# Optimization experiments

Hardware: AMD Instinct MI355X
Metric: run time of the kernel (lower is better)

## Reference

```python
import jax, jax.numpy as jnp
import numpy as np

K_NN = 9  # kernel_size: neighbors per node (includes self, dist 0)


def knn_edges(feat):
    """feat: (B, C, N). Replicates DenseDilatedKnnGraph (dilation=1):
    L2-normalize over channels, dense pairwise sq-distance, top-k nearest."""
    nrm = jnp.sqrt(jnp.sum(feat * feat, axis=1, keepdims=True))
    xn = feat / jnp.maximum(nrm, 1e-12)            # F.normalize(dim=1)
    xt = jnp.swapaxes(xn, 1, 2)                    # (B, N, C)
    sq = jnp.sum(xt * xt, axis=-1)                 # (B, N)
    dist = sq[:, :, None] + sq[:, None, :] - 2.0 * jnp.einsum('bnc,bmc->bnm', xt, xt)
    _, nn_idx = jax.lax.top_k(-dist, K_NN)         # (B, N, k)
    center = jnp.broadcast_to(jnp.arange(nn_idx.shape[1], dtype=nn_idx.dtype)[None, :, None], nn_idx.shape)
    return nn_idx, center                          # (x_j sources, x_i targets)


def reference(x, W0, W1, bias):
    B, C, H, W = x.shape
    N = H * W
    NB = B * N
    feat = x.reshape(B, C, N)
    # KNN graph is built on detached features in the torch source
    x_j, x_i = knn_edges(jax.lax.stop_gradient(feat))
    E = B * N * K_NN
    # faithful to source: torch.linspace(0, B, steps=E, dtype=int64) batch offsets
    count = jnp.linspace(0.0, float(B), E).astype(jnp.int32)
    src = x_j.reshape(-1).astype(jnp.int32) + count * N
    dst = x_i.reshape(-1).astype(jnp.int32) + count * N
    valid = (src < NB) & (dst < NB)                # drop the out-of-range tail edge
    # flat_nodes: (B, C, H, W) -> (B*H*W, C), node id = b*HW + pixel
    nodes = jnp.swapaxes(feat, 1, 2).reshape(NB, C)
    # ChebConv K=2, sym norm, lambda_max=2: Tx0 = x, Tx1 = -(D^-1/2 A D^-1/2) x
    w = valid.astype(nodes.dtype)
    deg = jax.ops.segment_sum(w, src, num_segments=NB)
    dinv = jnp.where(deg > 0, jax.lax.rsqrt(jnp.maximum(deg, 1.0)), 0.0)
    norm = -(dinv[src] * w * dinv[dst])            # scaled-Laplacian edge weights
    msg = norm[:, None] * nodes[src]               # (E, C) gather + weight
    Tx1 = jax.ops.segment_sum(msg, dst, num_segments=NB)
    return nodes @ W0 + Tx1 @ W1 + bias


def setup_inputs() -> dict:
    key = jax.random.key(0)
    k1, k2, k3, k4 = jax.random.split(key, 4)
    B, C, H, W = 8, 48, 64, 64
    Cout = 48
    s = 1.0 / np.sqrt(C)
    return {
        'x': jax.random.normal(k1, (B, C, H, W), dtype=jnp.float32),
        'W0': jax.random.normal(k2, (C, Cout), dtype=jnp.float32) * s,
        'W1': jax.random.normal(k3, (C, Cout), dtype=jnp.float32) * s,
        'bias': jax.random.normal(k4, (Cout,), dtype=jnp.float32) * 0.01,
    }
```

## Files before the change

kernel.cpp:

```cpp
#include <hip/hip_runtime.h>

#define BATCH 8
#define CH    48
#define NPTS  4096
#define NBN   (BATCH*NPTS)
#define KNN   9
#define NCAND 12

typedef unsigned short u16;
typedef unsigned int   u32;
typedef unsigned long long u64;
typedef __bf16 bf16x8 __attribute__((ext_vector_type(8)));
typedef float  f32x4  __attribute__((ext_vector_type(4)));

__device__ __forceinline__ float bf2f(u16 v) { return __uint_as_float(((u32)v) << 16); }
__device__ __forceinline__ u16 f2bf(float f) {
  u32 u = __float_as_uint(f);
  u = (u + 0x7fffu + ((u >> 16) & 1u)) >> 16;
  return (u16)u;
}

#define MED3U(d, a, b, c) \
  asm("v_med3_u32 %0, %1, %2, %3" : "=v"(d) : "v"(a), "v"(b), "v"(c))
#define INS12(p0,p1,p2,p3,p4,p5,p6,p7,p8,p9,p10,p11,x) do { \
  MED3U(p11,p10,p11,x); MED3U(p10,p9,p10,x); MED3U(p9,p8,p9,x);  \
  MED3U(p8, p7, p8, x); MED3U(p7, p6,p7, x); MED3U(p6,p5,p6,x);  \
  MED3U(p5, p4, p5, x); MED3U(p4, p3,p4, x); MED3U(p3,p2,p3,x);  \
  MED3U(p2, p1, p2, x); MED3U(p1, p0,p1, x); p0 = min(p0, x);    \
} while (0)

__device__ __forceinline__ void stage_q(const u16* g, u16* l) {
  __builtin_amdgcn_global_load_lds(
      (const __attribute__((address_space(1))) void*)g,
      (__attribute__((address_space(3))) void*)l, 16, 0, 0);
}

__global__ __launch_bounds__(256)
void k_prep(const float* __restrict__ x, float* __restrict__ xraw,
            float* __restrict__ xn, float* __restrict__ csq,
            u16* __restrict__ Abuf, u16* __restrict__ Bbuf,
            int* __restrict__ deg) {
  int node = blockIdx.x * 256 + threadIdx.x;
  deg[node] = 0;
  int b = node >> 12, n = node & (NPTS - 1);
  const float* xb = x + (size_t)b * CH * NPTS;
  float f[CH];
#pragma unroll
  for (int c = 0; c < CH; ++c) f[c] = xb[(size_t)c * NPTS + n];
  float a0 = 0, a1 = 0, a2 = 0, a3 = 0;
#pragma unroll
  for (int k = 0; k < CH; k += 4) {
    a0 += f[k] * f[k]; a1 += f[k+1] * f[k+1];
    a2 += f[k+2] * f[k+2]; a3 += f[k+3] * f[k+3];
  }
  float nrm = fmaxf(sqrtf((a0 + a1) + (a2 + a3)), 1e-12f);
  float xv[CH];
#pragma unroll
  for (int c = 0; c < CH; ++c) xv[c] = f[c] / nrm;
  a0 = a1 = a2 = a3 = 0;
#pragma unroll
  for (int k = 0; k < CH; k += 4) {
    a0 += xv[k] * xv[k]; a1 += xv[k+1] * xv[k+1];
    a2 += xv[k+2] * xv[k+2]; a3 += xv[k+3] * xv[k+3];
  }
  float csqv = (a0 + a1) + (a2 + a3);
  csq[node] = csqv;
  float4* ro = (float4*)(xraw + (size_t)node * CH);
  float4* no = (float4*)(xn   + (size_t)node * CH);
#pragma unroll
  for (int i = 0; i < CH / 4; ++i) {
    ro[i] = make_float4(f[4*i], f[4*i+1], f[4*i+2], f[4*i+3]);
    no[i] = make_float4(xv[4*i], xv[4*i+1], xv[4*i+2], xv[4*i+3]);
  }
  u16 ah[64], al[64];
#pragma unroll
  for (int k = 0; k < CH; ++k) {
    float av = -2.0f * xv[k];
    u16 h = f2bf(av); ah[k] = h; al[k] = f2bf(av - bf2f(h));
  }
  { u16 h = f2bf(csqv); ah[48] = h; al[48] = f2bf(csqv - bf2f(h)); }
#pragma unroll
  for (int k = 49; k < 64; ++k) { ah[k] = 0; al[k] = 0; }
  u16* Bh = Bbuf + (size_t)node * 128;
#pragma unroll
  for (int k = 0; k < CH; ++k) {
    float bv = xv[k];
    u16 h = f2bf(bv); Bh[k] = h; Bh[64 + k] = f2bf(bv - bf2f(h));
  }
  Bh[48] = 0x3F80; Bh[64 + 48] = 0;
#pragma unroll
  for (int k = 49; k < 64; ++k) { Bh[k] = 0; Bh[64 + k] = 0; }
  u16* Ag = Abuf + (size_t)(node >> 4) * 2048 + (size_t)(node & 15) * 8;
#pragma unroll
  for (int v = 0; v < 4; ++v) {
    const u16* src = (v < 2) ? ah : al;
    int koff = (v & 1) * 32;
#pragma unroll
    for (int q = 0; q < 4; ++q) {
      uint4 pk;
      const u16* s = src + koff + q * 8;
      pk.x = (u32)s[0] | ((u32)s[1] << 16);
      pk.y = (u32)s[2] | ((u32)s[3] << 16);
      pk.z = (u32)s[4] | ((u32)s[5] << 16);
      pk.w = (u32)s[6] | ((u32)s[7] << 16);
      *(uint4*)(Ag + v * 512 + q * 128) = pk;
    }
  }
}

__global__ __launch_bounds__(256, 6)
void k_knn_m(const u16* __restrict__ Abuf, const u16* __restrict__ Bbuf,
             u32* __restrict__ candu) {
  __shared__ __align__(16) u16 As[2][2048];
  int tid = threadIdx.x;
  int lane = tid & 63;
  int wv = tid >> 6;
  int quad = lane >> 4, m16 = lane & 15;
  int panel = blockIdx.x * 4 + wv;
  int row = panel * 16 + m16;
  int b4096 = row & ~(NPTS - 1);
  int quarter = blockIdx.y;
  int ct0 = quarter * 64;

  const __bf16* Bb = (const __bf16*)Bbuf + (size_t)row * 128;
  bf16x8 bh0 = *(const bf16x8*)(Bb + quad * 8);
  bf16x8 bh1 = *(const bf16x8*)(Bb + 32 + quad * 8);
  bf16x8 bl0 = *(const bf16x8*)(Bb + 64 + quad * 8);
  bf16x8 bl1 = *(const bf16x8*)(Bb + 96 + quad * 8);

  const u16* gs = Abuf + ((size_t)(b4096 >> 4) + ct0) * 2048
                  + wv * 512 + lane * 8;

  u32 s0=~0u,s1=~0u,s2=~0u,s3=~0u,s4=~0u,s5=~0u,
      s6=~0u,s7=~0u,s8=~0u,s9=~0u,s10=~0u,s11=~0u;

#define LDA(BUF, A0,A1,A2,A3) do {                                          \
    const u16* _p = &As[BUF][lane * 8];                                     \
    A0 = *(const bf16x8*)(_p);                                              \
    A1 = *(const bf16x8*)(_p + 512);                                        \
    A2 = *(const bf16x8*)(_p + 1024);                                       \
    A3 = *(const bf16x8*)(_p + 1536);                                       \
  } while (0)
#define MFMA6(ACC, A0,A1,A2,A3) do {                                        \
    ACC = (f32x4){2.5f, 2.5f, 2.5f, 2.5f};                                  \
    ACC = __builtin_amdgcn_mfma_f32_16x16x32_bf16(A0, bh0, ACC, 0, 0, 0);   \
    ACC = __builtin_amdgcn_mfma_f32_16x16x32_bf16(A1, bh1, ACC, 0, 0, 0);   \
    ACC = __builtin_amdgcn_mfma_f32_16x16x32_bf16(A0, bl0, ACC, 0, 0, 0);   \
    ACC = __builtin_amdgcn_mfma_f32_16x16x32_bf16(A1, bl1, ACC, 0, 0, 0);   \
    ACC = __builtin_amdgcn_mfma_f32_16x16x32_bf16(A2, bh0, ACC, 0, 0, 0);   \
    ACC = __builtin_amdgcn_mfma_f32_16x16x32_bf16(A3, bh1, ACC, 0, 0, 0);   \
  } while (0)
#define FILTER(ACC, CT) do {                                                \
    u32 _colb = ((u32)(CT) << 4) | ((u32)quad << 2);                        \
    _Pragma("unroll")                                                       \
    for (int _r = 0; _r < 4; ++_r) {                                        \
      u32 _u = __float_as_uint((ACC)[_r]);                                  \
      u32 _x = (_u & 0xFFFFF000u) | (_colb | (u32)_r);                      \
      INS12(s0,s1,s2,s3,s4,s5,s6,s7,s8,s9,s10,s11, _x);                     \
    }                                                                       \
  } while (0)

  f32x4 accA, accB;
  bf16x8 a0, a1, a2, a3;

  stage_q(gs, &As[0][wv * 512]);
  __syncthreads();

  LDA(0, a0, a1, a2, a3);
  stage_q(gs + (size_t)1 * 2048, &As[1][wv * 512]);
  MFMA6(accA, a0, a1, a2, a3);
  __syncthreads();

  for (int i = 0; i < 31; ++i) {
    int t = 2 * i + 1;
    LDA(1, a0, a1, a2, a3);
    stage_q(gs + (size_t)(t + 1) * 2048, &As[0][wv * 512]);
    FILTER(accA, ct0 + t - 1);
    MFMA6(accB, a0, a1, a2, a3);
    __syncthreads();
    LDA(0, a0, a1, a2, a3);
    stage_q(gs + (size_t)(t + 2) * 2048, &As[1][wv * 512]);
    FILTER(accB, ct0 + t);
    MFMA6(accA, a0, a1, a2, a3);
    __syncthreads();
  }
  LDA(1, a0, a1, a2, a3);
  FILTER(accA, ct0 + 62);
  MFMA6(accB, a0, a1, a2, a3);
  FILTER(accB, ct0 + 63);
#undef LDA
#undef MFMA6
#undef FILTER

  u32* o = candu + (((size_t)row * 4 + quarter) * 4 + quad) * NCAND;
  o[0]=s0; o[1]=s1; o[2]=s2; o[3]=s3; o[4]=s4; o[5]=s5;
  o[6]=s6; o[7]=s7; o[8]=s8; o[9]=s9; o[10]=s10; o[11]=s11;
}

__global__ __launch_bounds__(256, 4)
void k_reduce(const u32* __restrict__ candu, u32* __restrict__ cand12) {
  __shared__ u32 ls[64 * 4 * NCAND];
  int tid = threadIdx.x;
  int lr = tid >> 2, q = tid & 3;
  int row = blockIdx.x * 64 + lr;
  const u32* src = candu + (size_t)row * 192 + q * 48;
  u32 t0=~0u,t1=~0u,t2=~0u,t3=~0u,t4=~0u,t5=~0u,
      t6=~0u,t7=~0u,t8=~0u,t9=~0u,t10=~0u,t11=~0u;
  for (int s = 0; s < 48; ++s) {
    u32 x = src[s];
    INS12(t0,t1,t2,t3,t4,t5,t6,t7,t8,t9,t10,t11, x);
  }
  u32* lw = ls + (size_t)(lr * 4 + q) * NCAND;
  lw[0]=t0; lw[1]=t1; lw[2]=t2; lw[3]=t3; lw[4]=t4; lw[5]=t5;
  lw[6]=t6; lw[7]=t7; lw[8]=t8; lw[9]=t9; lw[10]=t10; lw[11]=t11;
  __syncthreads();
  if (q == 0) {
    u32 g0=~0u,g1=~0u,g2=~0u,g3=~0u,g4=~0u,g5=~0u,
        g6=~0u,g7=~0u,g8=~0u,g9=~0u,g10=~0u,g11=~0u;
    const u32* lsrc = ls + (size_t)lr * 48;
    for (int s = 0; s < 48; ++s) {
      u32 x = lsrc[s];
      INS12(g0,g1,g2,g3,g4,g5,g6,g7,g8,g9,g10,g11, x);
    }
    u32* o = cand12 + (size_t)row * NCAND;
    o[0]=(g0&0xFFFu); o[1]=(g1&0xFFFu); o[2]=(g2&0xFFFu);
    o[3]=(g3&0xFFFu); o[4]=(g4&0xFFFu); o[5]=(g5&0xFFFu);
    o[6]=(g6&0xFFFu); o[7]=(g7&0xFFFu); o[8]=(g8&0xFFFu);
    o[9]=(g9&0xFFFu); o[10]=(g10&0xFFFu); o[11]=(g11&0xFFFu);
  }
}

#define RR 16
__global__ __launch_bounds__(256, 4)
void k_rescore(const float* __restrict__ xn, const float* __restrict__ csq,
               const u32* __restrict__ cand12,
               u16* __restrict__ nn, int* __restrict__ deg) {
  __shared__ float dS[RR * NCAND];
  __shared__ int   iS[RR * NCAND];
  int tid = threadIdx.x;
  int lr = tid >> 4, q = tid & 15;
  int bi = blockIdx.x;
  int row = (bi & 7) * NPTS + (bi >> 3) * RR + lr;
  int b4096 = row & ~(NPTS - 1);
  const float* xnb = xn + (size_t)b4096 * CH;
  if (q < NCAND) {
    float rf[CH];
    const float4* p = (const float4*)(xn + (size_t)row * CH);
#pragma unroll
    for (int i = 0; i < CH / 4; ++i) {
      float4 v = p[i];
      rf[4*i] = v.x; rf[4*i+1] = v.y; rf[4*i+2] = v.z; rf[4*i+3] = v.w;
    }
    float sqn = csq[row];
    int c = (int)(cand12[(size_t)row * NCAND + q] & (NPTS - 1));
    const float4* cp = (const float4*)(xnb + (size_t)c * CH);
    float a0 = 0, a1 = 0, a2 = 0, a3 = 0;
#pragma unroll
    for (int i = 0; i < CH / 4; ++i) {
      float4 v = cp[i];
      a0 += rf[4*i]   * v.x; a1 += rf[4*i+1] * v.y;
      a2 += rf[4*i+2] * v.z; a3 += rf[4*i+3] * v.w;
    }
    float dist = (sqn + csq[b4096 + c]) - 2.0f * ((a0 + a1) + (a2 + a3));
    dS[lr * NCAND + q] = dist;
    iS[lr * NCAND + q] = c;
  }
  __syncthreads();
  if (q == 0) {
    float gd[KNN]; int gi[KNN];
#pragma unroll
    for (int j = 0; j < KNN; ++j) { gd[j] = 3.4e38f; gi[j] = 0x7fffffff; }
    for (int s = 0; s < NCAND; ++s) {
      float dc = dS[lr * NCAND + s]; int ic = iS[lr * NCAND + s];
      if (dc < gd[KNN - 1] || (dc == gd[KNN - 1] && ic < gi[KNN - 1])) {
        gd[KNN - 1] = dc; gi[KNN - 1] = ic;
#pragma unroll
        for (int k2 = KNN - 1; k2 > 0; --k2) {
          bool sw = (gd[k2] < gd[k2 - 1]) ||
                    (gd[k2] == gd[k2 - 1] && gi[k2] < gi[k2 - 1]);
          if (sw) {
            float td = gd[k2]; gd[k2] = gd[k2 - 1]; gd[k2 - 1] = td;
            int ti = gi[k2]; gi[k2] = gi[k2 - 1]; gi[k2 - 1] = ti;
          }
        }
      }
    }
    u16* o = nn + (size_t)row * KNN;
    int jmax = (row == NBN - 1) ? (KNN - 1) : KNN;
#pragma unroll
    for (int j = 0; j < KNN; ++j) o[j] = (u16)(gi[j] & (NPTS - 1));
    for (int j = 0; j < jmax; ++j)
      atomicAdd(&deg[b4096 + (gi[j] & (NPTS - 1))], 1);
  }
}

#define ONB 64
#define LPAD 52
__global__ __launch_bounds__(256)
void k_out_f(const float* __restrict__ xraw, const u16* __restrict__ nn,
             const int* __restrict__ deg,
             const float* __restrict__ W0, const float* __restrict__ W1,
             const float* __restrict__ bias, float* __restrict__ out) {
  __shared__ float w0[CH * CH], w1[CH * CH], bs[CH];
  __shared__ __align__(16) float fS[ONB * LPAD];
  __shared__ __align__(16) float txS[ONB * LPAD];
  __shared__ float dinvS[ONB];
  int tid = threadIdx.x;
  int bi = blockIdx.x;
  int n0 = (bi & 7) * NPTS + (bi >> 3) * ONB;
  int b12 = n0 & ~(NPTS - 1);
  for (int i = tid; i < CH * CH; i += 256) { w0[i] = W0[i]; w1[i] = W1[i]; }
  if (tid < CH) bs[tid] = bias[tid];
  for (int i = tid; i < ONB * 12; i += 256) {
    int ln = i / 12, f4 = i % 12;
    *(float4*)(fS + ln * LPAD + f4 * 4) =
        *(const float4*)(xraw + (size_t)(n0 + ln) * CH + f4 * 4);
  }
  if (tid < ONB) {
    int dg = deg[n0 + tid];
    dinvS[tid] = (dg > 0) ? (1.0f / sqrtf((float)dg)) : 0.0f;
  }
  __syncthreads();

  int ln = tid >> 2, p = tid & 3;
  int node = n0 + ln;
  float dn = dinvS[ln];
  const u16* nrow = nn + (size_t)node * KNN;
  bool full = (node != NBN - 1);
  float tx[12];
#pragma unroll
  for (int i = 0; i < 12; ++i) tx[i] = 0.f;
#pragma unroll
  for (int j = 0; j < KNN; ++j) {
    if (j < KNN - 1 || full) {
      int s = nrow[j] & (NPTS - 1);
      int dgs = deg[b12 + s];
      float ds = (dgs > 0) ? (1.0f / sqrtf((float)dgs)) : 0.0f;
      float w = -(ds * dn);
      const float4* pr = (const float4*)(xraw + (size_t)(b12 + s) * CH + p * 12);
#pragma unroll
      for (int q3 = 0; q3 < 3; ++q3) {
        float4 v = pr[q3];
        tx[q3*4]   += w * v.x; tx[q3*4+1] += w * v.y;
        tx[q3*4+2] += w * v.z; tx[q3*4+3] += w * v.w;
      }
    }
  }
#pragma unroll
  for (int q3 = 0; q3 < 3; ++q3)
    *(float4*)(txS + ln * LPAD + p * 12 + q3 * 4) =
        make_float4(tx[q3*4], tx[q3*4+1], tx[q3*4+2], tx[q3*4+3]);
  __syncthreads();

  float acc[12];
#pragma unroll
  for (int i = 0; i < 12; ++i) acc[i] = bs[p * 12 + i];
  const float* fr = fS + ln * LPAD;
  const float* tr = txS + ln * LPAD;
#pragma unroll
  for (int c = 0; c < CH; ++c) {
    float fc = fr[c];
    const float* wr = w0 + c * CH + p * 12;
#pragma unroll
    for (int i = 0; i < 12; ++i) acc[i] += fc * wr[i];
  }
#pragma unroll
  for (int c = 0; c < CH; ++c) {
    float tc = tr[c];
    const float* wr = w1 + c * CH + p * 12;
#pragma unroll
    for (int i = 0; i < 12; ++i) acc[i] += tc * wr[i];
  }
  float* op = out + (size_t)node * CH + p * 12;
#pragma unroll
  for (int q3 = 0; q3 < 3; ++q3)
    *(float4*)(op + q3 * 4) =
        make_float4(acc[q3*4], acc[q3*4+1], acc[q3*4+2], acc[q3*4+3]);
}

__global__ __launch_bounds__(256)
void k_zero(int* __restrict__ deg) { deg[blockIdx.x * 256 + threadIdx.x] = 0; }

__global__ __launch_bounds__(256)
void k_hist(const u16* __restrict__ nn, int* __restrict__ deg) {
  int node = blockIdx.x * 256 + threadIdx.x;
  int b12 = node & ~(NPTS - 1);
  int jmax = (node == NBN - 1) ? (KNN - 1) : KNN;
  for (int j = 0; j < jmax; ++j)
    atomicAdd(&deg[b12 + (nn[(size_t)node * KNN + j] & (NPTS - 1))], 1);
}

__global__ __launch_bounds__(256)
void k_dinv(const int* __restrict__ deg, float* __restrict__ dinv) {
  int i = blockIdx.x * 256 + threadIdx.x;
  int dg = deg[i];
  dinv[i] = (dg > 0) ? (1.0f / sqrtf((float)dg)) : 0.0f;
}

#define NQ    4
#define QCOLS (NPTS/NQ)
#define TCOLS 32
#define NTILES (QCOLS/TCOLS)
#define RPB   64

__global__ __launch_bounds__(256)
void k_knn_nb(const float* __restrict__ x, u16* __restrict__ nn) {
  __shared__ __align__(16) float tile[NQ * TCOLS * CH];
  __shared__ float nrmS[NQ * TCOLS];
  __shared__ float csq[NQ * TCOLS];
  int tid = threadIdx.x;
  int r0 = blockIdx.x * RPB;
  int b  = r0 >> 12;
  int q  = tid >> 6;
  int lr = tid & 63;
  int n  = (r0 + lr) & (NPTS - 1);
  const float* xb = x + (size_t)b * CH * NPTS;
  float rf[CH];
#pragma unroll
  for (int c = 0; c < CH; ++c) rf[c] = xb[(size_t)c * NPTS + n];
  float sqn;
  {
    float a0 = 0, a1 = 0, a2 = 0, a3 = 0;
#pragma unroll
    for (int k = 0; k < CH; k += 4) {
      a0 += rf[k] * rf[k]; a1 += rf[k+1] * rf[k+1];
      a2 += rf[k+2] * rf[k+2]; a3 += rf[k+3] * rf[k+3];
    }
    float nrm = fmaxf(sqrtf((a0 + a1) + (a2 + a3)), 1e-12f);
#pragma unroll
    for (int c = 0; c < CH; ++c) rf[c] = rf[c] / nrm;
    a0 = a1 = a2 = a3 = 0;
#pragma unroll
    for (int k = 0; k < CH; k += 4) {
      a0 += rf[k] * rf[k]; a1 += rf[k+1] * rf[k+1];
      a2 += rf[k+2] * rf[k+2]; a3 += rf[k+3] * rf[k+3];
    }
    sqn = (a0 + a1) + (a2 + a3);
  }
  float d[KNN]; int id[KNN];
#pragma unroll
  for (int j = 0; j < KNN; ++j) { d[j] = 3.4e38f; id[j] = 0x7fffffff; }
  for (int t = 0; t < NTILES; ++t) {
    __syncthreads();
#pragma unroll
    for (int qq = 0; qq < NQ; ++qq) {
      int colbase = qq * QCOLS + t * TCOLS;
      float* dst = tile + qq * TCOLS * CH;
#pragma unroll
      for (int it = 0; it < 6; ++it) {
        int i = it * 256 + tid;
        int c = i >> 5, p = i & 31;
        dst[p * CH + c] = xb[(size_t)c * NPTS + colbase + p];
      }
    }
    __syncthreads();
    if (tid < NQ * TCOLS) {
      const float* cp = tile + tid * CH;
      float a0 = 0, a1 = 0, a2 = 0, a3 = 0;
#pragma unroll
      for (int k = 0; k < CH; k += 4) {
        float4 v = *(const float4*)(cp + k);
        a0 += v.x * v.x; a1 += v.y * v.y; a2 += v.z * v.z; a3 += v.w * v.w;
      }
      nrmS[tid] = fmaxf(sqrtf((a0 + a1) + (a2 + a3)), 1e-12f);
    }
    __syncthreads();
    for (int i = tid; i < NQ * TCOLS * CH; i += 256)
      tile[i] = tile[i] / nrmS[i / CH];
    __syncthreads();
    if (tid < NQ * TCOLS) {
      const float* cp = tile + tid * CH;
      float a0 = 0, a1 = 0, a2 = 0, a3 = 0;
#pragma unroll
      for (int k = 0; k < CH; k += 4) {
        float4 v = *(const float4*)(cp + k);
        a0 += v.x * v.x; a1 += v.y * v.y; a2 += v.z * v.z; a3 += v.w * v.w;
      }
      csq[tid] = (a0 + a1) + (a2 + a3);
    }
    __syncthreads();
    int cbase = q * QCOLS + t * TCOLS;
    const float* tq = tile + q * TCOLS * CH;
    for (int cc = 0; cc < TCOLS; ++cc) {
      const float* cp = tq + cc * CH;
      float a0 = 0, a1 = 0, a2 = 0, a3 = 0;
#pragma unroll
      for (int k = 0; k < CH; k += 4) {
        float4 v = *(const float4*)(cp + k);
        a0 += rf[k] * v.x; a1 += rf[k+1] * v.y;
        a2 += rf[k+2] * v.z; a3 += rf[k+3] * v.w;
      }
      float dist = (sqn + csq[q * TCOLS + cc]) - 2.0f * ((a0 + a1) + (a2 + a3));
      if (dist < d[KNN - 1]) {
        d[KNN - 1] = dist; id[KNN - 1] = cbase + cc;
#pragma unroll
        for (int k2 = KNN - 1; k2 > 0; --k2) {
          if (d[k2] < d[k2 - 1]) {
            float td = d[k2]; d[k2] = d[k2 - 1]; d[k2 - 1] = td;
            int ti = id[k2]; id[k2] = id[k2 - 1]; id[k2 - 1] = ti;
          }
        }
      }
    }
  }
  __syncthreads();
  float* md = tile;
  int*   mi = (int*)(tile + 256 * KNN);
#pragma unroll
  for (int j = 0; j < KNN; ++j) { md[tid * KNN + j] = d[j]; mi[tid * KNN + j] = id[j]; }
  __syncthreads();
  if (tid < RPB) {
    float fd[KNN]; int fi[KNN];
#pragma unroll
    for (int j = 0; j < KNN; ++j) { fd[j] = 3.4e38f; fi[j] = 0x7fffffff; }
    for (int qq = 0; qq < NQ; ++qq) {
      int s = qq * RPB + tid;
      for (int j = 0; j < KNN; ++j) {
        float dc = md[s * KNN + j]; int ic = mi[s * KNN + j];
        if (dc < fd[KNN - 1]) {
          fd[KNN - 1] = dc; fi[KNN - 1] = ic;
#pragma unroll
          for (int k2 = KNN - 1; k2 > 0; --k2) {
            if (fd[k2] < fd[k2 - 1]) {
              float td = fd[k2]; fd[k2] = fd[k2 - 1]; fd[k2 - 1] = td;
              int ti = fi[k2]; fi[k2] = fi[k2 - 1]; fi[k2 - 1] = ti;
            }
          }
        }
      }
    }
    u16* o = nn + (size_t)(r0 + tid) * KNN;
#pragma unroll
    for (int j = 0; j < KNN; ++j) o[j] = (u16)(fi[j] & (NPTS - 1));
  }
}

__global__ __launch_bounds__(256)
void k_out_nb(const float* __restrict__ x, const u16* __restrict__ nn,
              const float* __restrict__ dinv,
              const float* __restrict__ W0, const float* __restrict__ W1,
              const float* __restrict__ bias, float* __restrict__ out) {
  __shared__ float w0[CH * CH], w1[CH * CH], bs[CH];
  for (int i = threadIdx.x; i < CH * CH; i += 256) { w0[i] = W0[i]; w1[i] = W1[i]; }
  if (threadIdx.x < CH) bs[threadIdx.x] = bias[threadIdx.x];
  __syncthreads();
  int node = blockIdx.x * 256 + threadIdx.x;
  int b = node >> 12, n = node & (NPTS - 1);
  const float* xb = x + (size_t)b * CH * NPTS;
  float f[CH], acc[CH], tx[CH];
#pragma unroll
  for (int c = 0; c < CH; ++c) f[c] = xb[(size_t)c * NPTS + n];
#pragma unroll
  for (int o = 0; o < CH; ++o) acc[o] = bs[o];
#pragma unroll
  for (int c = 0; c < CH; ++c) {
    float fc = f[c];
    const float* wr = w0 + c * CH;
#pragma unroll
    for (int o = 0; o < CH; ++o) acc[o] += fc * wr[o];
  }
#pragma unroll
  for (int c = 0; c < CH; ++c) tx[c] = 0.f;
  float dn = dinv[node];
  int jmax = (node == NBN - 1) ? (KNN - 1) : KNN;
  for (int j = 0; j < jmax; ++j) {
    int s = nn[(size_t)node * KNN + j] & (NPTS - 1);
    float w = -(dinv[(b << 12) + s] * dn);
#pragma unroll
    for (int c = 0; c < CH; ++c) tx[c] += w * xb[(size_t)c * NPTS + s];
  }
#pragma unroll
  for (int c = 0; c < CH; ++c) {
    float tc = tx[c];
    const float* wr = w1 + c * CH;
#pragma unroll
    for (int o = 0; o < CH; ++o) acc[o] += tc * wr[o];
  }
  float4* op = (float4*)(out + (size_t)node * CH);
#pragma unroll
  for (int i = 0; i < CH / 4; ++i)
    op[i] = make_float4(acc[4*i], acc[4*i+1], acc[4*i+2], acc[4*i+3]);
}

extern "C" void kernel_launch(void* const* d_in, const int* in_sizes, int n_in,
                              void* d_out, int out_size, void* d_ws, size_t ws_size,
                              hipStream_t stream) {
  const float* x    = (const float*)d_in[0];
  const float* W0   = (const float*)d_in[1];
  const float* W1   = (const float*)d_in[2];
  const float* bias = (const float*)d_in[3];
  float* out = (float*)d_out;
  char* w = (char*)d_ws;

  const size_t SZ_XN   = (size_t)NBN * CH * 4;
  const size_t SZ_XRAW = (size_t)NBN * CH * 4;
  const size_t SZ_CSQ  = (size_t)NBN * 4;
  const size_t SZ_NN   = (size_t)NBN * KNN * 2;
  const size_t SZ_DEG  = (size_t)NBN * 4;
  const size_t SZ_AB   = (size_t)NBN * 128 * 2;
  const size_t SZ_CU   = (size_t)NBN * 16 * NCAND * 4;
  const size_t SZ_C12  = (size_t)NBN * NCAND * 4;
  const size_t needF = SZ_XN + SZ_XRAW + SZ_CSQ + SZ_NN + SZ_DEG
                     + 2 * SZ_AB + SZ_CU + SZ_C12;

  if (ws_size >= needF) {
    size_t off = 0;
    float* xn   = (float*)(w + off); off += SZ_XN;
    float* xraw = (float*)(w + off); off += SZ_XRAW;
    float* csq  = (float*)(w + off); off += SZ_CSQ;
    u16*   nn   = (u16*)  (w + off); off += SZ_NN;
    int*   deg  = (int*)  (w + off); off += SZ_DEG;
    u16*   Abuf = (u16*)  (w + off); off += SZ_AB;
    u16*   Bbuf = (u16*)  (w + off); off += SZ_AB;
    u32*   candu= (u32*)  (w + off); off += SZ_CU;
    u32*   cand12=(u32*)  (w + off);
    k_prep    <<<NBN / 256, 256, 0, stream>>>(x, xraw, xn, csq, Abuf, Bbuf, deg);
    k_knn_m   <<<dim3(NBN / 64, 4), 256, 0, stream>>>(Abuf, Bbuf, candu);
    k_reduce  <<<NBN / 64, 256, 0, stream>>>(candu, cand12);
    k_rescore <<<NBN / RR, 256, 0, stream>>>(xn, csq, cand12, nn, deg);
    k_out_f   <<<NBN / ONB, 256, 0, stream>>>(xraw, nn, deg, W0, W1, bias, out);
  } else {
    u16*   nn   = (u16*)w;
    int*   deg  = (int*)(w + SZ_NN);
    float* dinv = (float*)(w + SZ_NN + SZ_DEG);
    k_knn_nb <<<NBN / RPB, 256, 0, stream>>>(x, nn);
    k_zero   <<<NBN / 256, 256, 0, stream>>>(deg);
    k_hist   <<<NBN / 256, 256, 0, stream>>>(nn, deg);
    k_dinv   <<<NBN / 256, 256, 0, stream>>>(deg, dinv);
    k_out_nb <<<NBN / 256, 256, 0, stream>>>(x, nn, dinv, W0, W1, bias, out);
  }
}
```

Before: 213.9 us.

## Stage two column tiles per barrier in KNN MFMA loop and vectorize reduce loads

The KNN distance kernel now stages two 16-column tiles per buffer phase, doubling shared memory to 16KB per block and halving the number of __syncthreads. The MFMA chains are interleaved with the FILTER insertion of the other accumulator, so matrix-core work can overlap with the sorting-network ALU work. The reduce kernel reads candidates with 128-bit loads from global and shared memory instead of scalar loads. Extra LDS use could lower occupancy below the 6-block launch bound, and the new loop schedule may raise register pressure.

```diff
diff --git a/kernel.cpp b/kernel.cpp
--- a/kernel.cpp
+++ b/kernel.cpp
@@ -111,7 +111,7 @@
 __global__ __launch_bounds__(256, 6)
 void k_knn_m(const u16* __restrict__ Abuf, const u16* __restrict__ Bbuf,
              u32* __restrict__ candu) {
-  __shared__ __align__(16) u16 As[2][2048];
+  __shared__ __align__(16) u16 As[2][2][2048];
   int tid = threadIdx.x;
   int lane = tid & 63;
   int wv = tid >> 6;
@@ -134,16 +134,17 @@
   u32 s0=~0u,s1=~0u,s2=~0u,s3=~0u,s4=~0u,s5=~0u,
       s6=~0u,s7=~0u,s8=~0u,s9=~0u,s10=~0u,s11=~0u;
 
-#define LDA(BUF, A0,A1,A2,A3) do {                                          \
-    const u16* _p = &As[BUF][lane * 8];                                     \
+  const f32x4 C25 = {2.5f, 2.5f, 2.5f, 2.5f};
+
+#define LDA(P, S, A0,A1,A2,A3) do {                                         \
+    const u16* _p = &As[P][S][lane * 8];                                    \
     A0 = *(const bf16x8*)(_p);                                              \
     A1 = *(const bf16x8*)(_p + 512);                                        \
     A2 = *(const bf16x8*)(_p + 1024);                                       \
     A3 = *(const bf16x8*)(_p + 1536);                                       \
   } while (0)
 #define MFMA6(ACC, A0,A1,A2,A3) do {                                        \
-    ACC = (f32x4){2.5f, 2.5f, 2.5f, 2.5f};                                  \
-    ACC = __builtin_amdgcn_mfma_f32_16x16x32_bf16(A0, bh0, ACC, 0, 0, 0);   \
+    ACC = __builtin_amdgcn_mfma_f32_16x16x32_bf16(A0, bh0, C25, 0, 0, 0);   \
     ACC = __builtin_amdgcn_mfma_f32_16x16x32_bf16(A1, bh1, ACC, 0, 0, 0);   \
     ACC = __builtin_amdgcn_mfma_f32_16x16x32_bf16(A0, bl0, ACC, 0, 0, 0);   \
     ACC = __builtin_amdgcn_mfma_f32_16x16x32_bf16(A1, bl1, ACC, 0, 0, 0);   \
@@ -163,30 +164,37 @@
   f32x4 accA, accB;
   bf16x8 a0, a1, a2, a3;
 
-  stage_q(gs, &As[0][wv * 512]);
-  __syncthreads();
-
-  LDA(0, a0, a1, a2, a3);
-  stage_q(gs + (size_t)1 * 2048, &As[1][wv * 512]);
+  stage_q(gs,        &As[0][0][wv * 512]);
+  stage_q(gs + 2048, &As[0][1][wv * 512]);
+  __syncthreads();
+
+  LDA(0, 0, a0, a1, a2, a3);
+  stage_q(gs + (size_t)2 * 2048, &As[1][0][wv * 512]);
+  stage_q(gs + (size_t)3 * 2048, &As[1][1][wv * 512]);
   MFMA6(accA, a0, a1, a2, a3);
-  __syncthreads();
-
-  for (int i = 0; i < 31; ++i) {
-    int t = 2 * i + 1;
-    LDA(1, a0, a1, a2, a3);
-    stage_q(gs + (size_t)(t + 1) * 2048, &As[0][wv * 512]);
-    FILTER(accA, ct0 + t - 1);
+  LDA(0, 1, a0, a1, a2, a3);
+  MFMA6(accB, a0, a1, a2, a3);
+  FILTER(accA, ct0 + 0);
+  __syncthreads();
+
+  for (int p = 1; p < 31; ++p) {
+    int par = p & 1;
+    LDA(par, 0, a0, a1, a2, a3);
+    stage_q(gs + (size_t)(2 * p + 2) * 2048, &As[par ^ 1][0][wv * 512]);
+    stage_q(gs + (size_t)(2 * p + 3) * 2048, &As[par ^ 1][1][wv * 512]);
+    MFMA6(accA, a0, a1, a2, a3);
+    FILTER(accB, ct0 + 2 * p - 1);
+    LDA(par, 1, a0, a1, a2, a3);
     MFMA6(accB, a0, a1, a2, a3);
+    FILTER(accA, ct0 + 2 * p);
     __syncthreads();
-    LDA(0, a0, a1, a2, a3);
-    stage_q(gs + (size_t)(t + 2) * 2048, &As[1][wv * 512]);
-    FILTER(accB, ct0 + t);
-    MFMA6(accA, a0, a1, a2, a3);
-    __syncthreads();
-  }
-  LDA(1, a0, a1, a2, a3);
+  }
+  LDA(1, 0, a0, a1, a2, a3);
+  MFMA6(accA, a0, a1, a2, a3);
+  FILTER(accB, ct0 + 61);
+  LDA(1, 1, a0, a1, a2, a3);
+  MFMA6(accB, a0, a1, a2, a3);
   FILTER(accA, ct0 + 62);
-  MFMA6(accB, a0, a1, a2, a3);
   FILTER(accB, ct0 + 63);
 #undef LDA
 #undef MFMA6
@@ -199,16 +207,19 @@
 
 __global__ __launch_bounds__(256, 4)
 void k_reduce(const u32* __restrict__ candu, u32* __restrict__ cand12) {
-  __shared__ u32 ls[64 * 4 * NCAND];
+  __shared__ __align__(16) u32 ls[64 * 4 * NCAND];
   int tid = threadIdx.x;
   int lr = tid >> 2, q = tid & 3;
   int row = blockIdx.x * 64 + lr;
-  const u32* src = candu + (size_t)row * 192 + q * 48;
+  const uint4* src = (const uint4*)(candu + (size_t)row * 192 + q * 48);
   u32 t0=~0u,t1=~0u,t2=~0u,t3=~0u,t4=~0u,t5=~0u,
       t6=~0u,t7=~0u,t8=~0u,t9=~0u,t10=~0u,t11=~0u;
-  for (int s = 0; s < 48; ++s) {
-    u32 x = src[s];
-    INS12(t0,t1,t2,t3,t4,t5,t6,t7,t8,t9,t10,t11, x);
+  for (int s = 0; s < 12; ++s) {
+    uint4 v = src[s];
+    INS12(t0,t1,t2,t3,t4,t5,t6,t7,t8,t9,t10,t11, v.x);
+    INS12(t0,t1,t2,t3,t4,t5,t6,t7,t8,t9,t10,t11, v.y);
+    INS12(t0,t1,t2,t3,t4,t5,t6,t7,t8,t9,t10,t11, v.z);
+    INS12(t0,t1,t2,t3,t4,t5,t6,t7,t8,t9,t10,t11, v.w);
   }
   u32* lw = ls + (size_t)(lr * 4 + q) * NCAND;
   lw[0]=t0; lw[1]=t1; lw[2]=t2; lw[3]=t3; lw[4]=t4; lw[5]=t5;
@@ -217,10 +228,13 @@
   if (q == 0) {
     u32 g0=~0u,g1=~0u,g2=~0u,g3=~0u,g4=~0u,g5=~0u,
         g6=~0u,g7=~0u,g8=~0u,g9=~0u,g10=~0u,g11=~0u;
-    const u32* lsrc = ls + (size_t)lr * 48;
-    for (int s = 0; s < 48; ++s) {
-      u32 x = lsrc[s];
-      INS12(g0,g1,g2,g3,g4,g5,g6,g7,g8,g9,g10,g11, x);
+    const uint4* lsrc = (const uint4*)(ls + (size_t)lr * 48);
+    for (int s = 0; s < 12; ++s) {
+      uint4 v = lsrc[s];
+      INS12(g0,g1,g2,g3,g4,g5,g6,g7,g8,g9,g10,g11, v.x);
+      INS12(g0,g1,g2,g3,g4,g5,g6,g7,g8,g9,g10,g11, v.y);
+      INS12(g0,g1,g2,g3,g4,g5,g6,g7,g8,g9,g10,g11, v.z);
+      INS12(g0,g1,g2,g3,g4,g5,g6,g7,g8,g9,g10,g11, v.w);
     }
     u32* o = cand12 + (size_t)row * NCAND;
     o[0]=(g0&0xFFFu); o[1]=(g1&0xFFFu); o[2]=(g2&0xFFFu);
```

Result: faster. 208.2 us (-2.7%).
